# Optimization experiments

Measured on AMD Instinct MI355X. Metric: run time of the kernel, lower is better.

Reference implementation:

```python
import jax, jax.numpy as jnp
import numpy as np

IN_C, OUT_C, K, STRIDE, PAD = 128, 256, 3, 1, 1


def setup_inputs() -> dict:
    key = jax.random.key(0)
    kx, kw = jax.random.split(key)
    x = jax.random.normal(kx, (32, IN_C, 56, 56), dtype=jnp.float32)
    weight = jax.random.normal(kw, (OUT_C, IN_C, K, K), dtype=jnp.float32) * 0.02
    bias = jnp.zeros((OUT_C,), dtype=jnp.float32)
    return {"x": x, "weight": weight, "bias": bias}


def reference(x, weight, bias):
    # Faithful conv2d: zero-pad + im2col + GEMM in the torch module is
    # mathematically a standard cross-correlation conv; use the fused primitive.
    out = jax.lax.conv_general_dilated(
        x, weight,
        window_strides=(STRIDE, STRIDE),
        padding=[(PAD, PAD), (PAD, PAD)],
        dimension_numbers=("NCHW", "OIHW", "NCHW"),
    )
    out = out + bias[None, :, None, None]
    return out
```

## Files before the change

### kernel.cpp

```cpp
#include <hip/hip_runtime.h>


typedef __attribute__((ext_vector_type(8))) short short8;
typedef __attribute__((ext_vector_type(4))) float f32x4;
typedef unsigned short ushort_t;

#define HWSZ 56
#define HW2 3136
#define INC 128
#define OUTC 256
#define NPIX 100352
#define PADW 58
#define XT_ELEMS 13778944
#define XT_BYTES 27557888

__device__ __forceinline__ ushort_t f2b(float f) {
    union { float f; unsigned u; } v; v.f = f;
    unsigned r = v.u + 0x7fffu + ((v.u >> 16) & 1u);
    return (ushort_t)(r >> 16);
}

__device__ __forceinline__ void glds16(const void* g, void* l) {
    __builtin_amdgcn_global_load_lds(
        (const __attribute__((address_space(1))) unsigned*)g,
        (__attribute__((address_space(3))) unsigned*)l, 16, 0, 0);
}

__global__ __launch_bounds__(256) void xt_kernel(const float* __restrict__ x,
                                                 ushort_t* __restrict__ xt) {
    __shared__ float tile[128][65];
    const int b = blockIdx.x;
    const int n = b / 49;
    const int hw0 = (b - n * 49) * 64;
    const int t = threadIdx.x;

    const float* xp = x + (size_t)n * (INC * HW2) + hw0;
    const int c_base = t >> 4;
    const int hwo = (t & 15) * 4;
#pragma unroll
    for (int j = 0; j < 8; ++j) {
        const int c = j * 16 + c_base;
        const f32x4 v = *reinterpret_cast<const f32x4*>(xp + c * HW2 + hwo);
        tile[c][hwo + 0] = v[0];
        tile[c][hwo + 1] = v[1];
        tile[c][hwo + 2] = v[2];
        tile[c][hwo + 3] = v[3];
    }
    __syncthreads();
    const int hw = t >> 2;
    const int q = t & 3;
    const int P = hw0 + hw;
    const int oh = P / HWSZ;
    const int ow = P - oh * HWSZ;
    ushort_t* dst = xt + (((size_t)n * PADW + oh + 1) * PADW + (ow + 1)) * INC;
#pragma unroll
    for (int g = 0; g < 4; ++g) {
        short8 v;
#pragma unroll
        for (int e = 0; e < 8; ++e) v[e] = (short)f2b(tile[g * 32 + q * 8 + e][hw]);
        *reinterpret_cast<short8*>(dst + g * 32 + q * 8) = v;
    }
}

__global__ __launch_bounds__(256) void wt_kernel(const float* __restrict__ w,
                                                 ushort_t* __restrict__ wt2) {
    const int tid = blockIdx.x * 256 + threadIdx.x;
    const int panel = tid >> 9;
    const int s = tid & 511;
    const int oc_tile = panel / 36;
    const int rem = panel - oc_tile * 36;
    const int pos = rem >> 2;
    const int icc = rem & 3;
    const int row = s >> 2;
    const int fq = (s & 3) ^ ((row >> 1) & 3);
    const int oc = oc_tile * 128 + row;
    const int ic0 = icc * 32 + fq * 8;
    short8 v;
#pragma unroll
    for (int e = 0; e < 8; ++e) v[e] = (short)f2b(w[(oc * 128 + ic0 + e) * 9 + pos]);
    *reinterpret_cast<short8*>(wt2 + (size_t)tid * 8) = v;
}

__global__ __launch_bounds__(256, 2) void conv_main(const ushort_t* __restrict__ xt,
                                                    const ushort_t* __restrict__ wt2,
                                                    const float* __restrict__ bias,
                                                    float* __restrict__ out) {
    __shared__ ushort_t lds[2][2][4096];

    const int bid = blockIdx.x;
    const int work = (bid & 7) * 196 + (bid >> 3);
    const int oc_tile = work & 1;
    const int P0 = (work >> 1) * 128;

    const int t = threadIdx.x;
    const int w = t >> 6;
    const int l = t & 63;
    const int fr = l & 15;
    const int fq = l >> 4;
    const int wr = w >> 1;
    const int wc = w & 1;

    const ushort_t* Abase = wt2 + (size_t)oc_tile * (36 * 4096) + t * 8;

    const int pa = w * 16 + (l >> 2);
    const int Pa = P0 + pa;
    const int na = Pa / HW2; const int hwa = Pa - na * HW2;
    const int oha = hwa / HWSZ; const int owa = hwa - oha * HWSZ;
    const int Pb = Pa + 64;
    const int nb = Pb / HW2; const int hwb = Pb - nb * HW2;
    const int ohb = hwb / HWSZ; const int owb = hwb - ohb * HWSZ;
    const ushort_t* xra = xt + (((size_t)na * PADW + oha) * PADW + owa) * INC;
    const ushort_t* xrb = xt + (((size_t)nb * PADW + ohb) * PADW + owb) * INC;
    const int swz = ((l & 3) ^ ((l >> 3) & 3)) * 8;

    const int frag_off = fr * 32 + ((fq ^ ((fr >> 1) & 3)) * 8);

    f32x4 acc[4][4];
#pragma unroll
    for (int i = 0; i < 4; ++i)
#pragma unroll
        for (int j = 0; j < 4; ++j) { f32x4 z = {0.f,0.f,0.f,0.f}; acc[i][j] = z; }

    glds16(Abase,            &lds[0][0][w * 512]);
    glds16(Abase + 2048,     &lds[0][0][(w + 4) * 512]);
    glds16(xra + swz,        &lds[0][1][w * 512]);
    glds16(xrb + swz,        &lds[0][1][(w + 4) * 512]);
    __syncthreads();

    int cur = 0;
    for (int s = 0; s < 36; ++s) {
        if (s < 35) {
            const int s1 = s + 1;
            const int pos = s1 >> 2;
            const int icc = s1 & 3;
            const int kh = pos / 3;
            const int kw = pos - kh * 3;
            const int koff = (kh * PADW + kw) * INC + icc * 32;
            const ushort_t* Ab = Abase + s1 * 4096;
            glds16(Ab,               &lds[cur ^ 1][0][w * 512]);
            glds16(Ab + 2048,        &lds[cur ^ 1][0][(w + 4) * 512]);
            glds16(xra + koff + swz, &lds[cur ^ 1][1][w * 512]);
            glds16(xrb + koff + swz, &lds[cur ^ 1][1][(w + 4) * 512]);
        }
        const ushort_t* A = &lds[cur][0][0];
        const ushort_t* B = &lds[cur][1][0];
        short8 af[4], bf[4];
#pragma unroll
        for (int mi = 0; mi < 4; ++mi)
            af[mi] = *reinterpret_cast<const short8*>(A + wr * 2048 + mi * 512 + frag_off);
#pragma unroll
        for (int ni = 0; ni < 4; ++ni)
            bf[ni] = *reinterpret_cast<const short8*>(B + wc * 2048 + ni * 512 + frag_off);
#pragma unroll
        for (int mi = 0; mi < 4; ++mi)
#pragma unroll
            for (int ni = 0; ni < 4; ++ni)
                acc[mi][ni] = __builtin_amdgcn_mfma_f32_16x16x32_bf16(af[mi], bf[ni],
                                                                      acc[mi][ni], 0, 0, 0);
        __syncthreads();
        cur ^= 1;
    }

    const int oc0 = oc_tile * 128;
    float bmr[4][4];
#pragma unroll
    for (int mi = 0; mi < 4; ++mi)
#pragma unroll
        for (int r = 0; r < 4; ++r)
            bmr[mi][r] = bias[oc0 + wr * 64 + mi * 16 + fq * 4 + r];

#pragma unroll
    for (int ni = 0; ni < 4; ++ni) {
        const int Pp = P0 + wc * 64 + ni * 16 + fr;
        const int nn = Pp / HW2;
        const int hwp = Pp - nn * HW2;
        float* op = out + (size_t)nn * (OUTC * HW2) + hwp;
#pragma unroll
        for (int mi = 0; mi < 4; ++mi)
#pragma unroll
            for (int r = 0; r < 4; ++r) {
                const int oc = oc0 + wr * 64 + mi * 16 + fq * 4 + r;
                op[oc * HW2] = acc[mi][ni][r] + bmr[mi][r];
            }
    }
}

extern "C" void kernel_launch(void* const* d_in, const int* in_sizes, int n_in,
                              void* d_out, int out_size, void* d_ws, size_t ws_size,
                              hipStream_t stream) {
    const float* x = (const float*)d_in[0];
    const float* w = (const float*)d_in[1];
    const float* bias = (const float*)d_in[2];
    float* out = (float*)d_out;

    ushort_t* xt = (ushort_t*)d_ws;
    ushort_t* wt2 = xt + XT_ELEMS;

    hipMemsetAsync(d_ws, 0, XT_BYTES, stream);
    xt_kernel<<<1568, 256, 0, stream>>>(x, xt);
    wt_kernel<<<144, 256, 0, stream>>>(w, wt2);
    conv_main<<<1568, 256, 0, stream>>>(xt, wt2, bias, out);
}
```

Measured before the change: 204.3 us.

## Triple-buffer conv LDS pipeline, zero only halo instead of full memset

Replaces the full workspace memset with a small kernel that zeroes only the padding border of the transposed input, since xt_kernel overwrites the interior. The main conv loop moves from double to triple buffering with two stages in flight, using explicit vmcnt waits plus a barrier instead of __syncthreads. It also raises MFMA issue priority and sets launch bounds to 3 blocks per CU. The extra LDS buffer (48KB per block) and the hand-written waitcnt could limit occupancy or introduce ordering hazards.

Measured after the change: 203.4 us. About the same (-0.4%).

```diff
diff --git a/kernel.cpp b/kernel.cpp
--- a/kernel.cpp
+++ b/kernel.cpp
@@ -9,10 +9,8 @@
 #define HW2 3136
 #define INC 128
 #define OUTC 256
-#define NPIX 100352
 #define PADW 58
 #define XT_ELEMS 13778944
-#define XT_BYTES 27557888
 
 __device__ __forceinline__ ushort_t f2b(float f) {
     union { float f; unsigned u; } v; v.f = f;
@@ -24,6 +22,21 @@
     __builtin_amdgcn_global_load_lds(
         (const __attribute__((address_space(1))) unsigned*)g,
         (__attribute__((address_space(3))) unsigned*)l, 16, 0, 0);
+}
+
+__global__ __launch_bounds__(256) void halo_zero(ushort_t* __restrict__ xt) {
+    const int tid = blockIdx.x * 256 + threadIdx.x;
+    const int g = tid & 15;
+    const int p = tid >> 4;
+    const int n = p / 228;
+    const int bp = p - n * 228;
+    int h, wv;
+    if (bp < 58)       { h = 0;        wv = bp; }
+    else if (bp < 116) { h = 57;       wv = bp - 58; }
+    else if (bp < 172) { h = bp - 115; wv = 0; }
+    else               { h = bp - 171; wv = 57; }
+    const short8 z = {0,0,0,0,0,0,0,0};
+    *reinterpret_cast<short8*>(xt + (((size_t)n * PADW + h) * PADW + wv) * INC + g * 8) = z;
 }
 
 __global__ __launch_bounds__(256) void xt_kernel(const float* __restrict__ x,
@@ -81,11 +94,11 @@
     *reinterpret_cast<short8*>(wt2 + (size_t)tid * 8) = v;
 }
 
-__global__ __launch_bounds__(256, 2) void conv_main(const ushort_t* __restrict__ xt,
+__global__ __launch_bounds__(256, 3) void conv_main(const ushort_t* __restrict__ xt,
                                                     const ushort_t* __restrict__ wt2,
                                                     const float* __restrict__ bias,
                                                     float* __restrict__ out) {
-    __shared__ ushort_t lds[2][2][4096];
+    __shared__ ushort_t lds[3][2][4096];
 
     const int bid = blockIdx.x;
     const int work = (bid & 7) * 196 + (bid >> 3);
@@ -121,29 +134,22 @@
 #pragma unroll
         for (int j = 0; j < 4; ++j) { f32x4 z = {0.f,0.f,0.f,0.f}; acc[i][j] = z; }
 
-    glds16(Abase,            &lds[0][0][w * 512]);
-    glds16(Abase + 2048,     &lds[0][0][(w + 4) * 512]);
-    glds16(xra + swz,        &lds[0][1][w * 512]);
-    glds16(xrb + swz,        &lds[0][1][(w + 4) * 512]);
-    __syncthreads();
-
-    int cur = 0;
-    for (int s = 0; s < 36; ++s) {
-        if (s < 35) {
-            const int s1 = s + 1;
-            const int pos = s1 >> 2;
-            const int icc = s1 & 3;
-            const int kh = pos / 3;
-            const int kw = pos - kh * 3;
-            const int koff = (kh * PADW + kw) * INC + icc * 32;
-            const ushort_t* Ab = Abase + s1 * 4096;
-            glds16(Ab,               &lds[cur ^ 1][0][w * 512]);
-            glds16(Ab + 2048,        &lds[cur ^ 1][0][(w + 4) * 512]);
-            glds16(xra + koff + swz, &lds[cur ^ 1][1][w * 512]);
-            glds16(xrb + koff + swz, &lds[cur ^ 1][1][(w + 4) * 512]);
-        }
-        const ushort_t* A = &lds[cur][0][0];
-        const ushort_t* B = &lds[cur][1][0];
+    auto stage = [&](int s1, int bsel) {
+        const int pos = s1 >> 2;
+        const int icc = s1 & 3;
+        const int kh = pos / 3;
+        const int kw = pos - kh * 3;
+        const int koff = (kh * PADW + kw) * INC + icc * 32;
+        const ushort_t* Ab = Abase + s1 * 4096;
+        glds16(Ab,               &lds[bsel][0][w * 512]);
+        glds16(Ab + 2048,        &lds[bsel][0][(w + 4) * 512]);
+        glds16(xra + koff + swz, &lds[bsel][1][w * 512]);
+        glds16(xrb + koff + swz, &lds[bsel][1][(w + 4) * 512]);
+    };
+
+    auto compute = [&](int bsel) {
+        const ushort_t* A = &lds[bsel][0][0];
+        const ushort_t* B = &lds[bsel][1][0];
         short8 af[4], bf[4];
 #pragma unroll
         for (int mi = 0; mi < 4; ++mi)
@@ -151,15 +157,29 @@
 #pragma unroll
         for (int ni = 0; ni < 4; ++ni)
             bf[ni] = *reinterpret_cast<const short8*>(B + wc * 2048 + ni * 512 + frag_off);
+        __builtin_amdgcn_s_setprio(1);
 #pragma unroll
         for (int mi = 0; mi < 4; ++mi)
 #pragma unroll
             for (int ni = 0; ni < 4; ++ni)
                 acc[mi][ni] = __builtin_amdgcn_mfma_f32_16x16x32_bf16(af[mi], bf[ni],
                                                                       acc[mi][ni], 0, 0, 0);
-        __syncthreads();
-        cur ^= 1;
-    }
+        __builtin_amdgcn_s_setprio(0);
+    };
+
+    stage(0, 0);
+    stage(1, 1);
+
+    int bc = 0, bn = 2;
+    for (int s = 0; s < 35; ++s) {
+        asm volatile("s_waitcnt vmcnt(4)\n\ts_barrier" ::: "memory");
+        if (s < 34) stage(s + 2, bn);
+        compute(bc);
+        bc = (bc == 2) ? 0 : bc + 1;
+        bn = (bn == 2) ? 0 : bn + 1;
+    }
+    asm volatile("s_waitcnt vmcnt(0)\n\ts_barrier" ::: "memory");
+    compute(bc);
 
     const int oc0 = oc_tile * 128;
     float bmr[4][4];
@@ -196,7 +216,7 @@
     ushort_t* xt = (ushort_t*)d_ws;
     ushort_t* wt2 = xt + XT_ELEMS;
 
-    hipMemsetAsync(d_ws, 0, XT_BYTES, stream);
+    halo_zero<<<456, 256, 0, stream>>>(xt);
     xt_kernel<<<1568, 256, 0, stream>>>(x, xt);
     wt_kernel<<<144, 256, 0, stream>>>(w, wt2);
     conv_main<<<1568, 256, 0, stream>>>(xt, wt2, bias, out);
```
